# Performance work log

Measured on AMD Instinct MI355X. Metric: run time of the kernel, lower is better.

The kernel has to match this reference:

```python
import jax, jax.numpy as jnp
import numpy as np

B, T, M, H = 64, 256, 512, 256  # batch, seq_len, d_model, lstm hidden


def setup_inputs() -> dict:
    key = jax.random.key(0)
    ks = jax.random.split(key, 10)
    s = 0.05  # weight init scale
    return {
        "enc_inputs": jax.random.normal(ks[0], (B, T, M), jnp.float32),
        "y": jax.random.normal(ks[1], (B, T, 1), jnp.float32),
        "Wd_w": jax.random.normal(ks[2], (M, 2 * H), jnp.float32) * s,  # W_d: Linear(2H, M)
        "Wd_b": jnp.zeros((M,), jnp.float32),
        "Ud_w": jax.random.normal(ks[3], (M, M), jnp.float32) * s,      # U_d: Linear(M, M, bias=False)
        "vd_w": jax.random.normal(ks[4], (1, M), jnp.float32) * s,      # v_d: Linear(M, 1, bias=False)
        "wt_w": jax.random.normal(ks[5], (1, M + 1), jnp.float32) * s,  # w_tilda: Linear(M+1, 1)
        "wt_b": jnp.zeros((1,), jnp.float32),
        "Wih": jax.random.normal(ks[6], (4 * H, 1), jnp.float32) * s,   # LSTMCell input weights
        "Whh": jax.random.normal(ks[7], (4 * H, H), jnp.float32) * s,   # LSTMCell hidden weights
        "bih": jnp.zeros((4 * H,), jnp.float32),
        "bhh": jnp.zeros((4 * H,), jnp.float32),
    }


def reference(enc_inputs, y, Wd_w, Wd_b, Ud_w, vd_w, wt_w, wt_b, Wih, Whh, bih, bhh):
    # U_d(enc_inputs) is loop-invariant -> hoist (same math as recomputing each step)
    y1 = jnp.einsum('btm,nm->btn', enc_inputs, Ud_w)  # [B,T,M]

    def step(carry, y_t):
        d, s = carry  # d = h_{t-1} [B,H], s = c'_{t-1} [B,H]
        x1 = jnp.concatenate([d, s], axis=1) @ Wd_w.T + Wd_b          # [B,M]
        z1 = jnp.tanh(x1[:, None, :] + y1)                            # [B,T,M]
        l_it = jnp.einsum('btm,m->bt', z1, vd_w[0])                   # [B,T]
        beta = jax.nn.softmax(l_it, axis=1)                           # softmax over encoder steps
        c_t = jnp.einsum('bt,btm->bm', beta, enc_inputs)              # [B,M]
        y_tilda = jnp.concatenate([c_t, y_t], axis=1) @ wt_w.T + wt_b # [B,1]
        # torch LSTMCell: gate order i, f, g, o
        gates = y_tilda @ Wih.T + bih + d @ Whh.T + bhh               # [B,4H]
        i, f, g, o = jnp.split(gates, 4, axis=1)
        s_new = jax.nn.sigmoid(f) * s + jax.nn.sigmoid(i) * jnp.tanh(g)
        d_new = jax.nn.sigmoid(o) * jnp.tanh(s_new)
        return (d_new, s_new), c_t

    b = enc_inputs.shape[0]
    init = (jnp.zeros((b, H), enc_inputs.dtype), jnp.zeros((b, H), enc_inputs.dtype))
    _, cs = jax.lax.scan(step, init, jnp.swapaxes(y, 0, 1))  # cs: [T,B,M]
    return jnp.sum(cs, axis=0)  # tgt = sum_t c_t, [B,M]
```

## Files before the change

kernel.cpp:

```cpp
#include <hip/hip_runtime.h>

typedef unsigned short u16;
typedef unsigned int u32;
typedef __attribute__((ext_vector_type(8))) short short8v;
typedef __attribute__((ext_vector_type(4))) float f32x4;
typedef __attribute__((ext_vector_type(4))) unsigned int u32x4;

#define NB 64
#define NT 256
#define NM 512
#define NH 256

#define K2 2.8853900817779268f
#define LOG2E 1.4426950408889634f

__device__ __forceinline__ float bf2f(u16 u) {
  union { unsigned i; float f; } c; c.i = ((unsigned)u) << 16; return c.f;
}
__device__ __forceinline__ u16 f2bf(float f) {
  union { float fv; unsigned i; } c; c.fv = f;
  unsigned i = c.i;
  return (u16)((i + 0x7fffu + ((i >> 16) & 1u)) >> 16);
}
__device__ __forceinline__ float bits2f(u32 u) {
  union { unsigned i; float f; } c; c.i = u; return c.f;
}
__device__ __forceinline__ float tanh_fast(float x) {
  return 1.0f - 2.0f * __builtin_amdgcn_rcpf(1.0f + __builtin_amdgcn_exp2f(K2 * x));
}
__device__ __forceinline__ float sigmoid_fast(float x) {
  return __builtin_amdgcn_rcpf(1.0f + __builtin_amdgcn_exp2f(-LOG2E * x));
}

__device__ __forceinline__ float unc_ld1(const float* p) {
  float r;
  asm volatile("global_load_dword %0, %1, off sc0 sc1\n\ts_waitcnt vmcnt(0)"
               : "=&v"(r) : "v"(p) : "memory");
  return r;
}
__device__ __forceinline__ void unc_ld1x4(const float* p0, const float* p1,
                                          const float* p2, const float* p3,
                                          float& a0, float& a1, float& a2, float& a3) {
  asm volatile(
      "global_load_dword %0, %4, off sc0 sc1\n\t"
      "global_load_dword %1, %5, off sc0 sc1\n\t"
      "global_load_dword %2, %6, off sc0 sc1\n\t"
      "global_load_dword %3, %7, off sc0 sc1\n\t"
      "s_waitcnt vmcnt(0)"
      : "=&v"(a0), "=&v"(a1), "=&v"(a2), "=&v"(a3)
      : "v"(p0), "v"(p1), "v"(p2), "v"(p3)
      : "memory");
}
__device__ __forceinline__ void unc_ld16f(const float* p, f32x4& a, f32x4& b,
                                          f32x4& c, f32x4& d) {
  asm volatile(
      "global_load_dwordx4 %0, %4, off sc0 sc1\n\t"
      "global_load_dwordx4 %1, %4, off offset:16 sc0 sc1\n\t"
      "global_load_dwordx4 %2, %4, off offset:32 sc0 sc1\n\t"
      "global_load_dwordx4 %3, %4, off offset:48 sc0 sc1\n\t"
      "s_waitcnt vmcnt(0)"
      : "=&v"(a), "=&v"(b), "=&v"(c), "=&v"(d)
      : "v"(p) : "memory");
}
__device__ __forceinline__ void unc_st1(float* p, float v) {
  asm volatile("global_store_dword %0, %1, off sc0 sc1" :: "v"(p), "v"(v) : "memory");
}
__device__ __forceinline__ void unc_st1u(u32* p, u32 v) {
  asm volatile("global_store_dword %0, %1, off sc0 sc1" :: "v"(p), "v"(v) : "memory");
}
__device__ __forceinline__ void unc_st4(float* p, f32x4 v) {
  asm volatile("global_store_dwordx4 %0, %1, off sc0 sc1" :: "v"(p), "v"(v) : "memory");
}
__device__ __forceinline__ void drain_vmem() {
  asm volatile("s_waitcnt vmcnt(0)" ::: "memory");
}
__device__ __forceinline__ void pollflags(const u32* p, u32 tg) {
  for (;;) {
    u32x4 f;
    asm volatile("global_load_dwordx4 %0, %1, off sc0 sc1\n\ts_waitcnt vmcnt(0)"
                 : "=&v"(f) : "v"(p) : "memory");
    if (f[0] >= tg && f[1] >= tg && f[2] >= tg && f[3] >= tg) break;
    __builtin_amdgcn_s_sleep(1);
  }
}

__global__ void convert_f32_bf16(const float* __restrict__ in, u16* __restrict__ out, int n) {
  int i = blockIdx.x * blockDim.x + threadIdx.x;
  if (i < n) out[i] = f2bf(in[i]);
}

__global__ __launch_bounds__(256) void gemm_y1(const u16* __restrict__ A,
                                               const u16* __restrict__ Bm,
                                               u16* __restrict__ C) {
  const int w = threadIdx.x >> 6;
  const int l = threadIdx.x & 63;
  const int kg = l >> 4;
  const int r16 = l & 15;
  const int rowbase = blockIdx.x * 64 + w * 16;
  const int colbase = blockIdx.y * 64;
  const u16* ap = A + (size_t)(rowbase + r16) * 512 + kg * 8;
  f32x4 acc0 = {0,0,0,0}, acc1 = {0,0,0,0}, acc2 = {0,0,0,0}, acc3 = {0,0,0,0};
  for (int k = 0; k < 512; k += 32) {
    short8v af = *(const short8v*)(ap + k);
    const u16* bp = Bm + (size_t)(colbase + r16) * 512 + kg * 8 + k;
    short8v b0 = *(const short8v*)(bp);
    short8v b1 = *(const short8v*)(bp + 16 * 512);
    short8v b2 = *(const short8v*)(bp + 32 * 512);
    short8v b3 = *(const short8v*)(bp + 48 * 512);
    acc0 = __builtin_amdgcn_mfma_f32_16x16x32_bf16(af, b0, acc0, 0, 0, 0);
    acc1 = __builtin_amdgcn_mfma_f32_16x16x32_bf16(af, b1, acc1, 0, 0, 0);
    acc2 = __builtin_amdgcn_mfma_f32_16x16x32_bf16(af, b2, acc2, 0, 0, 0);
    acc3 = __builtin_amdgcn_mfma_f32_16x16x32_bf16(af, b3, acc3, 0, 0, 0);
  }
  #pragma unroll
  for (int j = 0; j < 4; ++j) {
    int r = rowbase + (l >> 4) * 4 + j;
    C[(size_t)r * 512 + colbase +  0 + r16] = f2bf(K2 * acc0[j]);
    C[(size_t)r * 512 + colbase + 16 + r16] = f2bf(K2 * acc1[j]);
    C[(size_t)r * 512 + colbase + 32 + r16] = f2bf(K2 * acc2[j]);
    C[(size_t)r * 512 + colbase + 48 + r16] = f2bf(K2 * acc3[j]);
  }
}

__global__ __launch_bounds__(256) void wenc_kernel(const u16* __restrict__ encbf,
                                                   const float* __restrict__ wtw,
                                                   float* __restrict__ gwenc) {
  int b = blockIdx.x, te = threadIdx.x;
  const u16* ep = encbf + ((size_t)(b * NT + te)) * NM;
  float a = 0.0f;
  for (int c8 = 0; c8 < 64; ++c8) {
    short8v v = *(const short8v*)(ep + c8 * 8);
    #pragma unroll
    for (int jj = 0; jj < 8; ++jj) a = fmaf(bf2f((u16)v[jj]), wtw[c8 * 8 + jj], a);
  }
  gwenc[b * NT + te] = a;
}

__global__ __launch_bounds__(512) void bsum_kernel(const u16* __restrict__ encbf,
                                                   const float* __restrict__ gbeta,
                                                   float* __restrict__ out) {
  __shared__ float bl[NT];
  int b = blockIdx.x, m = threadIdx.x;
  if (m < 256) bl[m] = gbeta[b * NT + m];
  __syncthreads();
  const u16* ep = encbf + (size_t)b * NT * NM + m;
  float a = 0.0f;
  #pragma unroll 8
  for (int te = 0; te < NT; ++te)
    a = fmaf(bf2f(ep[(size_t)te * NM]), bl[te], a);
  out[b * NM + m] = a;
}

__attribute__((amdgpu_waves_per_eu(4, 4)))
__global__ void __launch_bounds__(1024) attn_scan(
    const u16* __restrict__ y1bf,
    const u16* __restrict__ whhbf,
    const u16* __restrict__ wdbf,
    const float* __restrict__ Wd_b,
    const float* __restrict__ vd,
    const float* __restrict__ wtw,
    const float* __restrict__ wtb,
    const float* __restrict__ Wih,
    const float* __restrict__ bih,
    const float* __restrict__ bhh,
    const float* __restrict__ yin,
    const float* __restrict__ gwenc,
    float* __restrict__ gx,
    float* __restrict__ st,
    u32* __restrict__ flags,
    float* __restrict__ gbeta)
{
  extern __shared__ char ldsraw[];
  u32* wdsl = (u32*)ldsraw;

  __shared__ float x1_l2[NM];
  __shared__ float d_l[NH];
  __shared__ float ds_f[128];
  __shared__ float l_sl[64];
  __shared__ float e_sl[64];
  __shared__ float whh_d_l[256];
  __shared__ float wih_l[256];
  __shared__ float bb_l[256];
  __shared__ float wenc_sl[64];
  __shared__ float yin_l[NT];
  __shared__ float merged[8];

  const int tid = threadIdx.x;
  const int bid = blockIdx.x;
  const int xcd = bid & 7, ii = bid >> 3;
  const int b = (xcd << 3) | (ii >> 2);
  const int q = ii & 3;
  const int w = tid >> 6, l = tid & 63;

  if (tid < 256) {
    int g = tid >> 6, h = tid & 63;
    int r = g * 256 + q * 64 + h;
    wih_l[tid] = Wih[r];
    bb_l[tid] = bih[r] + bhh[r];
    yin_l[tid] = yin[b * NT + tid];
  }
  if (tid < 64) wenc_sl[tid] = gwenc[b * NT + q * 64 + tid];

  float vr[8];
  #pragma unroll
  for (int j = 0; j < 8; ++j) vr[j] = vd[l * 8 + j];
  float sv = 0.0f;
  #pragma unroll
  for (int j = 0; j < 8; ++j) sv += vr[j];
  #pragma unroll
  for (int off = 32; off > 0; off >>= 1) sv += __shfl_xor(sv, off, 64);
  const float Svd = sv;
  const float wtw512 = wtw[NM];
  const float wtb0 = wtb[0];
  const float wdb_r = (tid < 512) ? Wd_b[tid] : 0.0f;

  u32x4 y1R0, y1R1, y1R2, y1R3;
  {
    const u16* base = y1bf + ((size_t)(b * NT + q * 64 + w * 4) << 9) + l * 8;
    y1R0 = *(const u32x4*)(base);
    y1R1 = *(const u32x4*)(base + 512);
    y1R2 = *(const u32x4*)(base + 1024);
    y1R3 = *(const u32x4*)(base + 1536);
  }
  asm volatile("" : "+v"(y1R0), "+v"(y1R1), "+v"(y1R2), "+v"(y1R3));

  {
    int m = tid >> 1, kh = tid & 1;
    for (int j = 0; j < 32; ++j) {
      int p = kh * 32 + j;
      int k0 = 2 * p, k1 = 2 * p + 1;
      int c0 = (k0 < 64) ? q * 64 + k0 : 256 + q * 64 + (k0 - 64);
      int c1 = (k1 < 64) ? q * 64 + k1 : 256 + q * 64 + (k1 - 64);
      u32 lo = wdbf[m * 512 + c0];
      u32 hi = wdbf[m * 512 + c1];
      int pg = (p >> 2) ^ (m & 15) ^ ((m >> 4) & 3);
      wdsl[m * 64 + pg * 4 + (p & 3)] = lo | (hi << 16);
    }
  }

  float s_reg = 0.0f;
  float bacc = 0.0f;
  __syncthreads();

  float* gxb = gx + b * 2304;
  float* stb = st + b * 16;
  u32* fS = flags + b * 32;
  u32* fP = flags + b * 32 + 8;

  #pragma unroll 1
  for (int t = 0; t < NT; ++t) {
    if (w == 15) pollflags(fP, (u32)t);
    __syncthreads();

    if (tid < 512) {
      const float* p = gxb + tid;
      float a0, a1, a2, a3;
      unc_ld1x4(p, p + 576, p + 1152, p + 1728, a0, a1, a2, a3);
      x1_l2[(tid & 7) * 64 + (tid >> 3)] = K2 * (wdb_r + ((a0 + a1) + (a2 + a3)));
    } else if (tid < 768) {
      int h = tid - 512;
      d_l[h] = unc_ld1(gxb + (h >> 6) * 576 + 512 + (h & 63));
    }
    __syncthreads();

    {
      float xr[8];
      #pragma unroll
      for (int j = 0; j < 8; ++j) xr[j] = x1_l2[j * 64 + l];
      auto lit = [&](u32x4 V, int idx) {
        float a = 0.0f;
        #pragma unroll
        for (int n = 0; n < 4; ++n) {
          u32 v = V[n];
          float e0 = __builtin_amdgcn_exp2f(xr[2 * n] + bits2f(v << 16));
          a = fmaf(vr[2 * n], __builtin_amdgcn_rcpf(1.0f + e0), a);
          float e1 = __builtin_amdgcn_exp2f(xr[2 * n + 1] + bits2f(v & 0xffff0000u));
          a = fmaf(vr[2 * n + 1], __builtin_amdgcn_rcpf(1.0f + e1), a);
        }
        #pragma unroll
        for (int off = 32; off > 0; off >>= 1) a += __shfl_xor(a, off, 64);
        if (l == 0) l_sl[w * 4 + idx] = Svd - 2.0f * a;
      };
      lit(y1R0, 0); lit(y1R1, 1); lit(y1R2, 2); lit(y1R3, 3);
    }
    __syncthreads();

    if (w == 0) {
      float v = l_sl[l];
      float mq = v;
      #pragma unroll
      for (int off = 32; off > 0; off >>= 1) mq = fmaxf(mq, __shfl_xor(mq, off, 64));
      float e = __builtin_amdgcn_exp2f((v - mq) * LOG2E);
      e_sl[l] = e;
      float sq = e, nq = e * wenc_sl[l];
      #pragma unroll
      for (int off = 32; off > 0; off >>= 1) {
        sq += __shfl_xor(sq, off, 64);
        nq += __shfl_xor(nq, off, 64);
      }
      if (l == 0) {
        f32x4 quad = {mq, sq, nq, 0.0f};
        unc_st4(stb + q * 4, quad);
        drain_vmem();
        unc_st1u(fS + q, (u32)(t + 1));
      }
    } else if (w <= 8) {
      #pragma unroll 1
      for (int pass = 0; pass < 2; ++pass) {
        int slot = (w - 1) * 64 + l + pass * 512;
        int rl = slot >> 2, kq = slot & 3;
        const u16* wr = whhbf + (size_t)((rl >> 6) * 256 + q * 64 + (rl & 63)) * 256 + kq * 64;
        float a = 0.0f;
        #pragma unroll
        for (int c8 = 0; c8 < 8; ++c8) {
          short8v wv = *(const short8v*)(wr + c8 * 8);
          #pragma unroll
          for (int jj = 0; jj < 8; ++jj)
            a = fmaf(bf2f((u16)wv[jj]), d_l[kq * 64 + c8 * 8 + jj], a);
        }
        a += __shfl_xor(a, 1, 64);
        a += __shfl_xor(a, 2, 64);
        if (kq == 0) whh_d_l[rl] = a;
      }
    } else if (w == 15) {
      pollflags(fS, (u32)(t + 1));
      f32x4 s0, s1, s2, s3;
      unc_ld16f(stb, s0, s1, s2, s3);
      float mx = fmaxf(fmaxf(s0[0], s1[0]), fmaxf(s2[0], s3[0]));
      float w0 = __builtin_amdgcn_exp2f((s0[0] - mx) * LOG2E);
      float w1 = __builtin_amdgcn_exp2f((s1[0] - mx) * LOG2E);
      float w2 = __builtin_amdgcn_exp2f((s2[0] - mx) * LOG2E);
      float w3 = __builtin_amdgcn_exp2f((s3[0] - mx) * LOG2E);
      float den = fmaf(s0[1], w0, fmaf(s1[1], w1, fmaf(s2[1], w2, s3[1] * w3)));
      float rden = __builtin_amdgcn_rcpf(den);
      float nsum = fmaf(s0[2], w0, fmaf(s1[2], w1, fmaf(s2[2], w2, s3[2] * w3)));
      float yt = nsum * rden + wtw512 * yin_l[t] + wtb0;
      if (l == 0) {
        merged[0] = yt; merged[1] = w0; merged[2] = w1;
        merged[3] = w2; merged[4] = w3; merged[5] = rden;
      }
    }
    __syncthreads();

    if (tid < 64) {
      float yt = merged[0];
      int h = tid;
      float gi = sigmoid_fast(whh_d_l[h]       + yt * wih_l[h]       + bb_l[h]);
      float gf = sigmoid_fast(whh_d_l[64 + h]  + yt * wih_l[64 + h]  + bb_l[64 + h]);
      float gg = tanh_fast   (whh_d_l[128 + h] + yt * wih_l[128 + h] + bb_l[128 + h]);
      float go = sigmoid_fast(whh_d_l[192 + h] + yt * wih_l[192 + h] + bb_l[192 + h]);
      float sn = gf * s_reg + gi * gg;
      s_reg = sn;
      float dn = go * tanh_fast(sn);
      ds_f[h] = dn;
      ds_f[64 + h] = sn;
      unc_st1(gxb + q * 576 + 512 + h, dn);
    } else if (w == 1) {
      float sc_q = merged[1 + q] * merged[5];
      bacc = fmaf(e_sl[l], sc_q, bacc);
    }
    __syncthreads();

    if (w < 8) {
      int m = w * 64 + l;
      const u32* row = wdsl + m * 64;
      const int sx = ((m & 15) ^ ((m >> 4) & 3)) << 2;
      float a = 0.0f;
      #pragma unroll
      for (int g = 0; g < 16; ++g) {
        u32x4 wv = *(const u32x4*)(row + ((g << 2) ^ sx));
        f32x4 d0 = *(const f32x4*)(ds_f + g * 8);
        f32x4 d1 = *(const f32x4*)(ds_f + g * 8 + 4);
        #pragma unroll
        for (int n = 0; n < 4; ++n) {
          u32 v = wv[n];
          float wlo = bits2f(v << 16);
          float whi = bits2f(v & 0xffff0000u);
          float dlo = (n < 2) ? d0[2 * n] : d1[2 * n - 4];
          float dhi = (n < 2) ? d0[2 * n + 1] : d1[2 * n - 3];
          a = fmaf(wlo, dlo, a);
          a = fmaf(whi, dhi, a);
        }
      }
      unc_st1(gxb + q * 576 + m, a);
    }
    drain_vmem();
    __syncthreads();
    if (tid == 0) unc_st1u(fP + q, (u32)(t + 1));
  }

  if (w == 1) gbeta[b * NT + q * 64 + l] = bacc;
}

extern "C" void kernel_launch(void* const* d_in, const int* in_sizes, int n_in,
                              void* d_out, int out_size, void* d_ws, size_t ws_size,
                              hipStream_t stream) {
  const float* enc  = (const float*)d_in[0];
  const float* yin  = (const float*)d_in[1];
  const float* Wd_w = (const float*)d_in[2];
  const float* Wd_b = (const float*)d_in[3];
  const float* Ud_w = (const float*)d_in[4];
  const float* vd_w = (const float*)d_in[5];
  const float* wt_w = (const float*)d_in[6];
  const float* wt_b = (const float*)d_in[7];
  const float* Wih  = (const float*)d_in[8];
  const float* Whh  = (const float*)d_in[9];
  const float* bih  = (const float*)d_in[10];
  const float* bhh  = (const float*)d_in[11];

  char* ws = (char*)d_ws;
  u16*   y1bf  = (u16*)(ws);
  u16*   encbf = (u16*)(ws + 16777216);
  u16*   udbf  = (u16*)(ws + 33554432);
  u16*   wdbf  = (u16*)(ws + 34078720);
  u16*   whhbf = (u16*)(ws + 34603008);
  float* gwenc = (float*)(ws + 35127296);
  float* gx    = (float*)(ws + 35192832);
  float* st    = (float*)(ws + 35782656);
  u32*   flags = (u32*)(ws + 35786752);
  float* gbeta = (float*)(ws + 35794944);

  hipMemsetAsync(ws + 35192832, 0, 602112, stream);

  convert_f32_bf16<<<8388608 / 256, 256, 0, stream>>>(enc, encbf, 8388608);
  convert_f32_bf16<<<262144 / 256, 256, 0, stream>>>(Ud_w, udbf, 262144);
  convert_f32_bf16<<<262144 / 256, 256, 0, stream>>>(Wd_w, wdbf, 262144);
  convert_f32_bf16<<<262144 / 256, 256, 0, stream>>>(Whh, whhbf, 262144);
  gemm_y1<<<dim3(256, 8), 256, 0, stream>>>(encbf, udbf, y1bf);
  wenc_kernel<<<64, 256, 0, stream>>>(encbf, wt_w, gwenc);

  hipFuncSetAttribute((const void*)attn_scan,
                      hipFuncAttributeMaxDynamicSharedMemorySize, 131072);
  attn_scan<<<256, 1024, 131072, stream>>>(y1bf, whhbf, wdbf, Wd_b, vd_w,
                                           wt_w, wt_b, Wih, bih, bhh, yin, gwenc,
                                           gx, st, flags, gbeta);
  bsum_kernel<<<64, 512, 0, stream>>>(encbf, gbeta, (float*)d_out);
}
```

Baseline: 4.235 ms.

## Run attention scan with one workgroup per batch instead of four cooperating

The recurrent scan changes from four workgroups per batch element, which synchronised every step through global-memory flags and uncached loads and stores, to a single 1024-thread workgroup per batch element that holds all 256 encoder steps of y1 in registers. The hidden and Wd matvecs now read transposed bf16 weights from global/L2, split across waves, with partial sums reduced through LDS. This removes the inter-workgroup polling and global round trips on each step. In exchange it uses only 64 workgroups, raises register pressure to 16 y1 vectors per thread, and streams the weights from cache every step instead of keeping Wd in LDS.

```diff
diff --git a/kernel.cpp b/kernel.cpp
--- a/kernel.cpp
+++ b/kernel.cpp
@@ -32,61 +32,22 @@
   return __builtin_amdgcn_rcpf(1.0f + __builtin_amdgcn_exp2f(-LOG2E * x));
 }
 
-__device__ __forceinline__ float unc_ld1(const float* p) {
-  float r;
-  asm volatile("global_load_dword %0, %1, off sc0 sc1\n\ts_waitcnt vmcnt(0)"
-               : "=&v"(r) : "v"(p) : "memory");
-  return r;
-}
-__device__ __forceinline__ void unc_ld1x4(const float* p0, const float* p1,
-                                          const float* p2, const float* p3,
-                                          float& a0, float& a1, float& a2, float& a3) {
-  asm volatile(
-      "global_load_dword %0, %4, off sc0 sc1\n\t"
-      "global_load_dword %1, %5, off sc0 sc1\n\t"
-      "global_load_dword %2, %6, off sc0 sc1\n\t"
-      "global_load_dword %3, %7, off sc0 sc1\n\t"
-      "s_waitcnt vmcnt(0)"
-      : "=&v"(a0), "=&v"(a1), "=&v"(a2), "=&v"(a3)
-      : "v"(p0), "v"(p1), "v"(p2), "v"(p3)
-      : "memory");
-}
-__device__ __forceinline__ void unc_ld16f(const float* p, f32x4& a, f32x4& b,
-                                          f32x4& c, f32x4& d) {
-  asm volatile(
-      "global_load_dwordx4 %0, %4, off sc0 sc1\n\t"
-      "global_load_dwordx4 %1, %4, off offset:16 sc0 sc1\n\t"
-      "global_load_dwordx4 %2, %4, off offset:32 sc0 sc1\n\t"
-      "global_load_dwordx4 %3, %4, off offset:48 sc0 sc1\n\t"
-      "s_waitcnt vmcnt(0)"
-      : "=&v"(a), "=&v"(b), "=&v"(c), "=&v"(d)
-      : "v"(p) : "memory");
-}
-__device__ __forceinline__ void unc_st1(float* p, float v) {
-  asm volatile("global_store_dword %0, %1, off sc0 sc1" :: "v"(p), "v"(v) : "memory");
-}
-__device__ __forceinline__ void unc_st1u(u32* p, u32 v) {
-  asm volatile("global_store_dword %0, %1, off sc0 sc1" :: "v"(p), "v"(v) : "memory");
-}
-__device__ __forceinline__ void unc_st4(float* p, f32x4 v) {
-  asm volatile("global_store_dwordx4 %0, %1, off sc0 sc1" :: "v"(p), "v"(v) : "memory");
-}
-__device__ __forceinline__ void drain_vmem() {
-  asm volatile("s_waitcnt vmcnt(0)" ::: "memory");
-}
-__device__ __forceinline__ void pollflags(const u32* p, u32 tg) {
-  for (;;) {
-    u32x4 f;
-    asm volatile("global_load_dwordx4 %0, %1, off sc0 sc1\n\ts_waitcnt vmcnt(0)"
-                 : "=&v"(f) : "v"(p) : "memory");
-    if (f[0] >= tg && f[1] >= tg && f[2] >= tg && f[3] >= tg) break;
-    __builtin_amdgcn_s_sleep(1);
-  }
-}
-
 __global__ void convert_f32_bf16(const float* __restrict__ in, u16* __restrict__ out, int n) {
   int i = blockIdx.x * blockDim.x + threadIdx.x;
   if (i < n) out[i] = f2bf(in[i]);
+}
+
+__global__ __launch_bounds__(256) void transpose_wd(const float* __restrict__ in,
+                                                    u16* __restrict__ out) {
+  int i = blockIdx.x * 256 + threadIdx.x;
+  int k = i >> 9, m = i & 511;
+  out[i] = f2bf(in[m * 512 + k]);
+}
+__global__ __launch_bounds__(256) void transpose_whh(const float* __restrict__ in,
+                                                     u16* __restrict__ out) {
+  int i = blockIdx.x * 256 + threadIdx.x;
+  int k = i >> 10, r = i & 1023;
+  out[i] = f2bf(in[r * 256 + k]);
 }
 
 __global__ __launch_bounds__(256) void gemm_y1(const u16* __restrict__ A,
@@ -151,11 +112,10 @@
   out[b * NM + m] = a;
 }
 
-__attribute__((amdgpu_waves_per_eu(4, 4)))
-__global__ void __launch_bounds__(1024) attn_scan(
+__global__ __launch_bounds__(1024) void attn_scan(
     const u16* __restrict__ y1bf,
-    const u16* __restrict__ whhbf,
-    const u16* __restrict__ wdbf,
+    const u16* __restrict__ wdt,
+    const u16* __restrict__ whht,
     const float* __restrict__ Wd_b,
     const float* __restrict__ vd,
     const float* __restrict__ wtw,
@@ -165,41 +125,39 @@
     const float* __restrict__ bhh,
     const float* __restrict__ yin,
     const float* __restrict__ gwenc,
-    float* __restrict__ gx,
-    float* __restrict__ st,
-    u32* __restrict__ flags,
     float* __restrict__ gbeta)
 {
   extern __shared__ char ldsraw[];
-  u32* wdsl = (u32*)ldsraw;
+  float* gp  = (float*)ldsraw;
+  float* x1p = (float*)(ldsraw + 32768);
 
   __shared__ float x1_l2[NM];
-  __shared__ float d_l[NH];
-  __shared__ float ds_f[128];
-  __shared__ float l_sl[64];
-  __shared__ float e_sl[64];
-  __shared__ float whh_d_l[256];
-  __shared__ float wih_l[256];
-  __shared__ float bb_l[256];
-  __shared__ float wenc_sl[64];
+  __shared__ float ds_l[NM];
+  __shared__ float l_sl[NT];
+  __shared__ float e_sl[NT];
+  __shared__ float wih_l[1024];
+  __shared__ float bb_l[1024];
+  __shared__ float wenc_l[NT];
   __shared__ float yin_l[NT];
-  __shared__ float merged[8];
+  __shared__ float wdb_l[NM];
+  __shared__ float merged[4];
 
   const int tid = threadIdx.x;
-  const int bid = blockIdx.x;
-  const int xcd = bid & 7, ii = bid >> 3;
-  const int b = (xcd << 3) | (ii >> 2);
-  const int q = ii & 3;
+  const int b = blockIdx.x;
   const int w = tid >> 6, l = tid & 63;
 
+  wih_l[tid] = Wih[tid];
+  bb_l[tid] = bih[tid] + bhh[tid];
   if (tid < 256) {
-    int g = tid >> 6, h = tid & 63;
-    int r = g * 256 + q * 64 + h;
-    wih_l[tid] = Wih[r];
-    bb_l[tid] = bih[r] + bhh[r];
+    wenc_l[tid] = gwenc[b * NT + tid];
     yin_l[tid] = yin[b * NT + tid];
   }
-  if (tid < 64) wenc_sl[tid] = gwenc[b * NT + q * 64 + tid];
+  if (tid < 512) {
+    float wb = Wd_b[tid];
+    wdb_l[tid] = wb;
+    x1_l2[(tid & 7) * 64 + (tid >> 3)] = K2 * wb;
+  }
+  for (int i = tid; i < 8192; i += 1024) gp[i] = 0.0f;
 
   float vr[8];
   #pragma unroll
@@ -212,66 +170,36 @@
   const float Svd = sv;
   const float wtw512 = wtw[NM];
   const float wtb0 = wtb[0];
-  const float wdb_r = (tid < 512) ? Wd_b[tid] : 0.0f;
-
-  u32x4 y1R0, y1R1, y1R2, y1R3;
+
+  u32x4 y1R[16];
   {
-    const u16* base = y1bf + ((size_t)(b * NT + q * 64 + w * 4) << 9) + l * 8;
-    y1R0 = *(const u32x4*)(base);
-    y1R1 = *(const u32x4*)(base + 512);
-    y1R2 = *(const u32x4*)(base + 1024);
-    y1R3 = *(const u32x4*)(base + 1536);
-  }
-  asm volatile("" : "+v"(y1R0), "+v"(y1R1), "+v"(y1R2), "+v"(y1R3));
-
-  {
-    int m = tid >> 1, kh = tid & 1;
-    for (int j = 0; j < 32; ++j) {
-      int p = kh * 32 + j;
-      int k0 = 2 * p, k1 = 2 * p + 1;
-      int c0 = (k0 < 64) ? q * 64 + k0 : 256 + q * 64 + (k0 - 64);
-      int c1 = (k1 < 64) ? q * 64 + k1 : 256 + q * 64 + (k1 - 64);
-      u32 lo = wdbf[m * 512 + c0];
-      u32 hi = wdbf[m * 512 + c1];
-      int pg = (p >> 2) ^ (m & 15) ^ ((m >> 4) & 3);
-      wdsl[m * 64 + pg * 4 + (p & 3)] = lo | (hi << 16);
-    }
-  }
+    const u16* ybase = y1bf + ((size_t)(b * NT + w * 16) << 9) + l * 8;
+    #pragma unroll
+    for (int i = 0; i < 16; ++i)
+      y1R[i] = *(const u32x4*)(ybase + (size_t)i * 512);
+  }
+  asm volatile("" : "+v"(y1R[0]), "+v"(y1R[1]), "+v"(y1R[2]), "+v"(y1R[3]),
+                    "+v"(y1R[4]), "+v"(y1R[5]), "+v"(y1R[6]), "+v"(y1R[7]),
+                    "+v"(y1R[8]), "+v"(y1R[9]), "+v"(y1R[10]), "+v"(y1R[11]),
+                    "+v"(y1R[12]), "+v"(y1R[13]), "+v"(y1R[14]), "+v"(y1R[15]));
 
   float s_reg = 0.0f;
   float bacc = 0.0f;
   __syncthreads();
 
-  float* gxb = gx + b * 2304;
-  float* stb = st + b * 16;
-  u32* fS = flags + b * 32;
-  u32* fP = flags + b * 32 + 8;
-
   #pragma unroll 1
   for (int t = 0; t < NT; ++t) {
-    if (w == 15) pollflags(fP, (u32)t);
-    __syncthreads();
-
-    if (tid < 512) {
-      const float* p = gxb + tid;
-      float a0, a1, a2, a3;
-      unc_ld1x4(p, p + 576, p + 1152, p + 1728, a0, a1, a2, a3);
-      x1_l2[(tid & 7) * 64 + (tid >> 3)] = K2 * (wdb_r + ((a0 + a1) + (a2 + a3)));
-    } else if (tid < 768) {
-      int h = tid - 512;
-      d_l[h] = unc_ld1(gxb + (h >> 6) * 576 + 512 + (h & 63));
-    }
-    __syncthreads();
-
     {
       float xr[8];
       #pragma unroll
       for (int j = 0; j < 8; ++j) xr[j] = x1_l2[j * 64 + l];
-      auto lit = [&](u32x4 V, int idx) {
+      float lout = 0.0f;
+      #pragma unroll
+      for (int i = 0; i < 16; ++i) {
         float a = 0.0f;
         #pragma unroll
         for (int n = 0; n < 4; ++n) {
-          u32 v = V[n];
+          u32 v = y1R[i][n];
           float e0 = __builtin_amdgcn_exp2f(xr[2 * n] + bits2f(v << 16));
           a = fmaf(vr[2 * n], __builtin_amdgcn_rcpf(1.0f + e0), a);
           float e1 = __builtin_amdgcn_exp2f(xr[2 * n + 1] + bits2f(v & 0xffff0000u));
@@ -279,117 +207,128 @@
         }
         #pragma unroll
         for (int off = 32; off > 0; off >>= 1) a += __shfl_xor(a, off, 64);
-        if (l == 0) l_sl[w * 4 + idx] = Svd - 2.0f * a;
-      };
-      lit(y1R0, 0); lit(y1R1, 1); lit(y1R2, 2); lit(y1R3, 3);
+        if (l == i) lout = Svd - 2.0f * a;
+      }
+      if (l < 16) l_sl[w * 16 + l] = lout;
     }
     __syncthreads();
 
     if (w == 0) {
-      float v = l_sl[l];
-      float mq = v;
-      #pragma unroll
-      for (int off = 32; off > 0; off >>= 1) mq = fmaxf(mq, __shfl_xor(mq, off, 64));
-      float e = __builtin_amdgcn_exp2f((v - mq) * LOG2E);
-      e_sl[l] = e;
-      float sq = e, nq = e * wenc_sl[l];
+      float v0 = l_sl[l], v1 = l_sl[64 + l], v2 = l_sl[128 + l], v3 = l_sl[192 + l];
+      float mx = fmaxf(fmaxf(v0, v1), fmaxf(v2, v3));
+      #pragma unroll
+      for (int off = 32; off > 0; off >>= 1) mx = fmaxf(mx, __shfl_xor(mx, off, 64));
+      float e0 = __builtin_amdgcn_exp2f((v0 - mx) * LOG2E);
+      float e1 = __builtin_amdgcn_exp2f((v1 - mx) * LOG2E);
+      float e2 = __builtin_amdgcn_exp2f((v2 - mx) * LOG2E);
+      float e3 = __builtin_amdgcn_exp2f((v3 - mx) * LOG2E);
+      e_sl[l] = e0; e_sl[64 + l] = e1; e_sl[128 + l] = e2; e_sl[192 + l] = e3;
+      float sq = ((e0 + e1) + (e2 + e3));
+      float nq = fmaf(e0, wenc_l[l], fmaf(e1, wenc_l[64 + l],
+                 fmaf(e2, wenc_l[128 + l], e3 * wenc_l[192 + l])));
       #pragma unroll
       for (int off = 32; off > 0; off >>= 1) {
         sq += __shfl_xor(sq, off, 64);
         nq += __shfl_xor(nq, off, 64);
       }
       if (l == 0) {
-        f32x4 quad = {mq, sq, nq, 0.0f};
-        unc_st4(stb + q * 4, quad);
-        drain_vmem();
-        unc_st1u(fS + q, (u32)(t + 1));
-      }
-    } else if (w <= 8) {
-      #pragma unroll 1
-      for (int pass = 0; pass < 2; ++pass) {
-        int slot = (w - 1) * 64 + l + pass * 512;
-        int rl = slot >> 2, kq = slot & 3;
-        const u16* wr = whhbf + (size_t)((rl >> 6) * 256 + q * 64 + (rl & 63)) * 256 + kq * 64;
-        float a = 0.0f;
-        #pragma unroll
-        for (int c8 = 0; c8 < 8; ++c8) {
-          short8v wv = *(const short8v*)(wr + c8 * 8);
-          #pragma unroll
-          for (int jj = 0; jj < 8; ++jj)
-            a = fmaf(bf2f((u16)wv[jj]), d_l[kq * 64 + c8 * 8 + jj], a);
-        }
-        a += __shfl_xor(a, 1, 64);
-        a += __shfl_xor(a, 2, 64);
-        if (kq == 0) whh_d_l[rl] = a;
-      }
-    } else if (w == 15) {
-      pollflags(fS, (u32)(t + 1));
-      f32x4 s0, s1, s2, s3;
-      unc_ld16f(stb, s0, s1, s2, s3);
-      float mx = fmaxf(fmaxf(s0[0], s1[0]), fmaxf(s2[0], s3[0]));
-      float w0 = __builtin_amdgcn_exp2f((s0[0] - mx) * LOG2E);
-      float w1 = __builtin_amdgcn_exp2f((s1[0] - mx) * LOG2E);
-      float w2 = __builtin_amdgcn_exp2f((s2[0] - mx) * LOG2E);
-      float w3 = __builtin_amdgcn_exp2f((s3[0] - mx) * LOG2E);
-      float den = fmaf(s0[1], w0, fmaf(s1[1], w1, fmaf(s2[1], w2, s3[1] * w3)));
-      float rden = __builtin_amdgcn_rcpf(den);
-      float nsum = fmaf(s0[2], w0, fmaf(s1[2], w1, fmaf(s2[2], w2, s3[2] * w3)));
-      float yt = nsum * rden + wtw512 * yin_l[t] + wtb0;
-      if (l == 0) {
-        merged[0] = yt; merged[1] = w0; merged[2] = w1;
-        merged[3] = w2; merged[4] = w3; merged[5] = rden;
-      }
-    }
-    __syncthreads();
-
-    if (tid < 64) {
+        float rden = __builtin_amdgcn_rcpf(sq);
+        merged[0] = nq * rden + wtw512 * yin_l[t] + wtb0;
+        merged[1] = rden;
+      }
+    }
+    __syncthreads();
+
+    if (tid < 256) {
       float yt = merged[0];
       int h = tid;
-      float gi = sigmoid_fast(whh_d_l[h]       + yt * wih_l[h]       + bb_l[h]);
-      float gf = sigmoid_fast(whh_d_l[64 + h]  + yt * wih_l[64 + h]  + bb_l[64 + h]);
-      float gg = tanh_fast   (whh_d_l[128 + h] + yt * wih_l[128 + h] + bb_l[128 + h]);
-      float go = sigmoid_fast(whh_d_l[192 + h] + yt * wih_l[192 + h] + bb_l[192 + h]);
+      float g0 = 0.0f, g1 = 0.0f, g2 = 0.0f, g3 = 0.0f;
+      #pragma unroll
+      for (int s = 0; s < 8; ++s) {
+        const float* gs = gp + s * 1024 + h;
+        g0 += gs[0]; g1 += gs[256]; g2 += gs[512]; g3 += gs[768];
+      }
+      float gi = sigmoid_fast(g0 + yt * wih_l[h]       + bb_l[h]);
+      float gf = sigmoid_fast(g1 + yt * wih_l[256 + h] + bb_l[256 + h]);
+      float gg = tanh_fast   (g2 + yt * wih_l[512 + h] + bb_l[512 + h]);
+      float go = sigmoid_fast(g3 + yt * wih_l[768 + h] + bb_l[768 + h]);
       float sn = gf * s_reg + gi * gg;
       s_reg = sn;
       float dn = go * tanh_fast(sn);
-      ds_f[h] = dn;
-      ds_f[64 + h] = sn;
-      unc_st1(gxb + q * 576 + 512 + h, dn);
-    } else if (w == 1) {
-      float sc_q = merged[1 + q] * merged[5];
-      bacc = fmaf(e_sl[l], sc_q, bacc);
+      ds_l[h] = dn;
+      ds_l[256 + h] = sn;
+    } else if (tid < 512) {
+      bacc = fmaf(e_sl[tid - 256], merged[1], bacc);
     }
     __syncthreads();
 
     if (w < 8) {
-      int m = w * 64 + l;
-      const u32* row = wdsl + m * 64;
-      const int sx = ((m & 15) ^ ((m >> 4) & 3)) << 2;
-      float a = 0.0f;
-      #pragma unroll
-      for (int g = 0; g < 16; ++g) {
-        u32x4 wv = *(const u32x4*)(row + ((g << 2) ^ sx));
-        f32x4 d0 = *(const f32x4*)(ds_f + g * 8);
-        f32x4 d1 = *(const f32x4*)(ds_f + g * 8 + 4);
-        #pragma unroll
-        for (int n = 0; n < 4; ++n) {
-          u32 v = wv[n];
-          float wlo = bits2f(v << 16);
-          float whi = bits2f(v & 0xffff0000u);
-          float dlo = (n < 2) ? d0[2 * n] : d1[2 * n - 4];
-          float dhi = (n < 2) ? d0[2 * n + 1] : d1[2 * n - 3];
-          a = fmaf(wlo, dlo, a);
-          a = fmaf(whi, dhi, a);
-        }
-      }
-      unc_st1(gxb + q * 576 + m, a);
-    }
-    drain_vmem();
-    __syncthreads();
-    if (tid == 0) unc_st1u(fP + q, (u32)(t + 1));
-  }
-
-  if (w == 1) gbeta[b * NT + q * 64 + l] = bacc;
+      float a0 = 0, a1 = 0, a2 = 0, a3 = 0, a4 = 0, a5 = 0, a6 = 0, a7 = 0;
+      const u16* base = wdt + (size_t)(w * 64) * 512 + l * 8;
+      const float* dsk = ds_l + w * 64;
+      #pragma unroll 8
+      for (int kk = 0; kk < 64; ++kk) {
+        u32x4 W = *(const u32x4*)(base + (size_t)kk * 512);
+        float dk = dsk[kk];
+        a0 = fmaf(bits2f(W[0] << 16), dk, a0);
+        a1 = fmaf(bits2f(W[0] & 0xffff0000u), dk, a1);
+        a2 = fmaf(bits2f(W[1] << 16), dk, a2);
+        a3 = fmaf(bits2f(W[1] & 0xffff0000u), dk, a3);
+        a4 = fmaf(bits2f(W[2] << 16), dk, a4);
+        a5 = fmaf(bits2f(W[2] & 0xffff0000u), dk, a5);
+        a6 = fmaf(bits2f(W[3] << 16), dk, a6);
+        a7 = fmaf(bits2f(W[3] & 0xffff0000u), dk, a7);
+      }
+      f32x4 o0 = {a0, a1, a2, a3}, o1 = {a4, a5, a6, a7};
+      *(f32x4*)(x1p + w * 512 + l * 8) = o0;
+      *(f32x4*)(x1p + w * 512 + l * 8 + 4) = o1;
+    } else {
+      const int sl = w - 8;
+      float a0 = 0, a1 = 0, a2 = 0, a3 = 0, a4 = 0, a5 = 0, a6 = 0, a7 = 0;
+      float c0 = 0, c1 = 0, c2 = 0, c3 = 0, c4 = 0, c5 = 0, c6 = 0, c7 = 0;
+      const u16* base = whht + (size_t)(sl * 32) * 1024 + l * 8;
+      const float* dsk = ds_l + sl * 32;
+      #pragma unroll 4
+      for (int kk = 0; kk < 32; ++kk) {
+        u32x4 Wa = *(const u32x4*)(base + (size_t)kk * 1024);
+        u32x4 Wb = *(const u32x4*)(base + (size_t)kk * 1024 + 512);
+        float dk = dsk[kk];
+        a0 = fmaf(bits2f(Wa[0] << 16), dk, a0);
+        a1 = fmaf(bits2f(Wa[0] & 0xffff0000u), dk, a1);
+        a2 = fmaf(bits2f(Wa[1] << 16), dk, a2);
+        a3 = fmaf(bits2f(Wa[1] & 0xffff0000u), dk, a3);
+        a4 = fmaf(bits2f(Wa[2] << 16), dk, a4);
+        a5 = fmaf(bits2f(Wa[2] & 0xffff0000u), dk, a5);
+        a6 = fmaf(bits2f(Wa[3] << 16), dk, a6);
+        a7 = fmaf(bits2f(Wa[3] & 0xffff0000u), dk, a7);
+        c0 = fmaf(bits2f(Wb[0] << 16), dk, c0);
+        c1 = fmaf(bits2f(Wb[0] & 0xffff0000u), dk, c1);
+        c2 = fmaf(bits2f(Wb[1] << 16), dk, c2);
+        c3 = fmaf(bits2f(Wb[1] & 0xffff0000u), dk, c3);
+        c4 = fmaf(bits2f(Wb[2] << 16), dk, c4);
+        c5 = fmaf(bits2f(Wb[2] & 0xffff0000u), dk, c5);
+        c6 = fmaf(bits2f(Wb[3] << 16), dk, c6);
+        c7 = fmaf(bits2f(Wb[3] & 0xffff0000u), dk, c7);
+      }
+      f32x4 o0 = {a0, a1, a2, a3}, o1 = {a4, a5, a6, a7};
+      f32x4 o2 = {c0, c1, c2, c3}, o3 = {c4, c5, c6, c7};
+      *(f32x4*)(gp + sl * 1024 + l * 8) = o0;
+      *(f32x4*)(gp + sl * 1024 + l * 8 + 4) = o1;
+      *(f32x4*)(gp + sl * 1024 + 512 + l * 8) = o2;
+      *(f32x4*)(gp + sl * 1024 + 512 + l * 8 + 4) = o3;
+    }
+    __syncthreads();
+
+    if (tid < 512) {
+      int m = tid;
+      float s = x1p[m] + x1p[512 + m] + x1p[1024 + m] + x1p[1536 + m]
+              + x1p[2048 + m] + x1p[2560 + m] + x1p[3072 + m] + x1p[3584 + m];
+      x1_l2[(m & 7) * 64 + (m >> 3)] = K2 * (wdb_l[m] + s);
+    }
+    __syncthreads();
+  }
+
+  if (tid >= 256 && tid < 512) gbeta[b * NT + (tid - 256)] = bacc;
 }
 
 extern "C" void kernel_launch(void* const* d_in, const int* in_sizes, int n_in,
@@ -409,30 +348,25 @@
   const float* bhh  = (const float*)d_in[11];
 
   char* ws = (char*)d_ws;
-  u16*   y1bf  = (u16*)(ws);
-  u16*   encbf = (u16*)(ws + 16777216);
-  u16*   udbf  = (u16*)(ws + 33554432);
-  u16*   wdbf  = (u16*)(ws + 34078720);
-  u16*   whhbf = (u16*)(ws + 34603008);
-  float* gwenc = (float*)(ws + 35127296);
-  float* gx    = (float*)(ws + 35192832);
-  float* st    = (float*)(ws + 35782656);
-  u32*   flags = (u32*)(ws + 35786752);
-  float* gbeta = (float*)(ws + 35794944);
-
-  hipMemsetAsync(ws + 35192832, 0, 602112, stream);
+  u16*   y1bf   = (u16*)(ws);
+  u16*   encbf  = (u16*)(ws + 16777216);
+  u16*   udbf   = (u16*)(ws + 33554432);
+  u16*   wdtbf  = (u16*)(ws + 34078720);
+  u16*   whhtbf = (u16*)(ws + 34603008);
+  float* gwenc  = (float*)(ws + 35127296);
+  float* gbeta  = (float*)(ws + 35192832);
 
   convert_f32_bf16<<<8388608 / 256, 256, 0, stream>>>(enc, encbf, 8388608);
   convert_f32_bf16<<<262144 / 256, 256, 0, stream>>>(Ud_w, udbf, 262144);
-  convert_f32_bf16<<<262144 / 256, 256, 0, stream>>>(Wd_w, wdbf, 262144);
-  convert_f32_bf16<<<262144 / 256, 256, 0, stream>>>(Whh, whhbf, 262144);
+  transpose_wd<<<1024, 256, 0, stream>>>(Wd_w, wdtbf);
+  transpose_whh<<<1024, 256, 0, stream>>>(Whh, whhtbf);
   gemm_y1<<<dim3(256, 8), 256, 0, stream>>>(encbf, udbf, y1bf);
   wenc_kernel<<<64, 256, 0, stream>>>(encbf, wt_w, gwenc);
 
   hipFuncSetAttribute((const void*)attn_scan,
-                      hipFuncAttributeMaxDynamicSharedMemorySize, 131072);
-  attn_scan<<<256, 1024, 131072, stream>>>(y1bf, whhbf, wdbf, Wd_b, vd_w,
-                                           wt_w, wt_b, Wih, bih, bhh, yin, gwenc,
-                                           gx, st, flags, gbeta);
+                      hipFuncAttributeMaxDynamicSharedMemorySize, 49152);
+  attn_scan<<<64, 1024, 49152, stream>>>(y1bf, wdtbf, whhtbf, Wd_b, vd_w,
+                                         wt_w, wt_b, Wih, bih, bhh, yin, gwenc,
+                                         gbeta);
   bsum_kernel<<<64, 512, 0, stream>>>(encbf, gbeta, (float*)d_out);
 }
```

After: 5.968 ms. 1.41x slower.
